# Kernel tuning notes

Measured on AMD Instinct MI355X. Metric: run time of the kernel, lower is better.

Reference implementation:

```python
import jax, jax.numpy as jnp
import numpy as np

N_NODES = 50000
N_EDGES = 800000
F_IN = 32
H = 128
N_REL = 4
MAX_DEG = 10
N_GRAPHS = 64
N_BLOCKS = 2


def setup_inputs() -> dict:
    key = jax.random.key(0)
    ks = jax.random.split(key, 20)
    s = 0.05
    return {
        "x": jax.random.normal(ks[0], (N_NODES, F_IN), jnp.float32),
        "edge_index": jax.random.randint(ks[1], (2, N_EDGES), 0, N_NODES, dtype=jnp.int32),
        "edge_attr": jax.random.randint(ks[2], (N_EDGES,), 0, N_REL, dtype=jnp.int32),
        "batch_idx": jnp.sort(jax.random.randint(ks[3], (N_NODES,), 0, N_GRAPHS, dtype=jnp.int32)),
        "embed_W": jax.random.normal(ks[4], (F_IN, H), jnp.float32) * s,
        "embed_b": jax.random.normal(ks[5], (H,), jnp.float32) * s,
        "rgcn_Wrel": jax.random.normal(ks[6], (N_BLOCKS, N_REL, H, H), jnp.float32) * s,
        "rgcn_Wroot": jax.random.normal(ks[7], (N_BLOCKS, H, H), jnp.float32) * s,
        "rgcn_b": jax.random.normal(ks[8], (N_BLOCKS, H), jnp.float32) * s,
        "mf_Wl": jax.random.normal(ks[9], (N_BLOCKS, MAX_DEG + 1, H, H), jnp.float32) * s,
        "mf_bl": jax.random.normal(ks[10], (N_BLOCKS, MAX_DEG + 1, H), jnp.float32) * s,
        "mf_Wr": jax.random.normal(ks[11], (N_BLOCKS, MAX_DEG + 1, H, H), jnp.float32) * s,
        "lin1_W": jax.random.normal(ks[12], (H, H), jnp.float32) * s,
        "lin1_b": jax.random.normal(ks[13], (H,), jnp.float32) * s,
        "lin2_W": jax.random.normal(ks[14], (H, 1), jnp.float32) * s,
        "lin2_b": jax.random.normal(ks[15], (1,), jnp.float32) * s,
    }


def _rgcn(x, src, dst, rel, Wrel, Wroot, b):
    # PyG RGCNConv with default aggr='mean': per-relation mean over incoming
    # edges, then per-relation weight, plus root transform and bias.
    seg = dst * N_REL + rel  # composite segment id: (node, relation)
    agg = jax.ops.segment_sum(x[src], seg, num_segments=N_NODES * N_REL)
    cnt = jax.ops.segment_sum(jnp.ones((seg.shape[0],), x.dtype), seg,
                              num_segments=N_NODES * N_REL)
    agg = (agg / jnp.maximum(cnt, 1.0)[:, None]).reshape(N_NODES, N_REL, H)
    return jnp.einsum('nrh,rho->no', agg, Wrel) + x @ Wroot + b


def _mfconv(x, src, dst, Wl, bl, Wr):
    # PyG MFConv: sum-aggregate neighbors, then per-degree-bucket linear heads
    # (degree = in-degree clamped to MAX_DEG); lin_r applied to root x (no bias).
    h = jax.ops.segment_sum(x[src], dst, num_segments=N_NODES)  # [N,H]
    deg = jax.ops.segment_sum(jnp.ones((src.shape[0],), jnp.int32), dst,
                              num_segments=N_NODES)
    deg = jnp.minimum(deg, MAX_DEG)  # [N]
    # out_all: [D+1, N, H] candidate outputs, one per degree bucket
    out_all = (jnp.einsum('nh,dho->dno', h, Wl)
               + jnp.einsum('nh,dho->dno', x, Wr)
               + bl[:, None, :])
    return jnp.take_along_axis(out_all, deg[None, :, None], axis=0)[0]


def reference(x, edge_index, edge_attr, batch_idx, embed_W, embed_b,
              rgcn_Wrel, rgcn_Wroot, rgcn_b, mf_Wl, mf_bl, mf_Wr,
              lin1_W, lin1_b, lin2_W, lin2_b):
    src, dst = edge_index[0], edge_index[1]
    h = x @ embed_W + embed_b
    for blk in range(N_BLOCKS):
        if blk > 0:  # first block uses Identity instead of ReLU
            h = jax.nn.relu(h)
        h = _rgcn(h, src, dst, edge_attr, rgcn_Wrel[blk], rgcn_Wroot[blk], rgcn_b[blk])
        h = jax.nn.relu(h)
        h = _mfconv(h, src, dst, mf_Wl[blk], mf_bl[blk], mf_Wr[blk])
    g = jax.ops.segment_sum(h, batch_idx, num_segments=N_GRAPHS)  # global_add_pool
    g = jax.nn.relu(g @ lin1_W + lin1_b)
    return g @ lin2_W + lin2_b
```

## Files before the change

kernel.cpp:

```cpp
#include <hip/hip_runtime.h>
#include <hip/hip_bf16.h>

#define NRELS 4
#define MAXDEG 10
#define NBUCK 11
#define POOL_CHUNKS 8

typedef __attribute__((ext_vector_type(8))) short s16x8;
typedef __attribute__((ext_vector_type(4))) float f32x4;
typedef __attribute__((ext_vector_type(8))) unsigned short u16x8;

__device__ inline unsigned short f2b(float f) {
  __hip_bfloat16 h = __float2bfloat16(f);
  return *reinterpret_cast<unsigned short*>(&h);
}
__device__ inline float b2f(unsigned short u) {
  union { unsigned int i; float f; } v;
  v.i = ((unsigned int)u) << 16;
  return v.f;
}
__device__ inline float blo(unsigned int v) {
  union { unsigned int i; float f; } x;
  x.i = v << 16;
  return x.f;
}
__device__ inline float bhi(unsigned int v) {
  union { unsigned int i; float f; } x;
  x.i = v & 0xffff0000u;
  return x.f;
}

typedef __attribute__((address_space(3))) unsigned int lds_uint;
typedef __attribute__((address_space(1))) const unsigned int glob_uint;
__device__ __forceinline__ void gld_lds16(const void* g, void* l) {
  __builtin_amdgcn_global_load_lds((glob_uint*)g, (lds_uint*)l, 16, 0, 0);
}

__global__ __launch_bounds__(512) void coarse_count_scan(
    const int* __restrict__ dst, int* __restrict__ bhist, int* __restrict__ boff,
    int* __restrict__ bcur, int* __restrict__ done, int NB, int E, int nblocks) {
  __shared__ int lh[512];
  __shared__ int lastf;
  int t = threadIdx.x;
  lh[t] = 0;
  __syncthreads();
  int base = blockIdx.x * 4096;
  int lim = E - base;
  if (lim > 4096) lim = 4096;
  for (int i = t; i < lim; i += 512) atomicAdd(&lh[dst[base + i] >> 7], 1);
  __syncthreads();
  if (lh[t]) atomicAdd(&bhist[t], lh[t]);
  __threadfence();
  __syncthreads();
  if (t == 0) lastf = (atomicAdd(done, 1) == nblocks - 1) ? 1 : 0;
  __syncthreads();
  if (!lastf) return;
  int v = (t < NB) ? atomicAdd(&bhist[t], 0) : 0;
  lh[t] = v;
  __syncthreads();
  for (int o = 1; o < 512; o <<= 1) {
    int x = (t >= o) ? lh[t - o] : 0;
    __syncthreads();
    lh[t] += x;
    __syncthreads();
  }
  if (t < NB) {
    int st = lh[t] - v;
    boff[t] = st;
    bcur[t] = st;
  }
  if (t == 0) boff[NB] = E;
}

__global__ __launch_bounds__(512) void coarse_scatter(
    const int* __restrict__ src, const int* __restrict__ dst, const int* __restrict__ rel,
    int* __restrict__ bcur, uint2* __restrict__ ebuf, int E) {
  __shared__ int lhist[512];
  __shared__ int lstart[512];
  __shared__ int lcur[512];
  __shared__ int gbase[512];
  __shared__ uint2 stage[4096];
  int t = threadIdx.x;
  lhist[t] = 0;
  __syncthreads();
  int base = blockIdx.x * 4096;
  int lim = E - base;
  if (lim > 4096) lim = 4096;
  for (int i = t; i < lim; i += 512) atomicAdd(&lhist[dst[base + i] >> 7], 1);
  __syncthreads();
  int myc = lhist[t];
  lstart[t] = myc;
  __syncthreads();
  for (int o = 1; o < 512; o <<= 1) {
    int x = (t >= o) ? lstart[t - o] : 0;
    __syncthreads();
    lstart[t] += x;
    __syncthreads();
  }
  int incl = lstart[t];
  __syncthreads();
  lstart[t] = incl - myc;
  lcur[t] = 0;
  if (myc > 0) gbase[t] = atomicAdd(&bcur[t], myc);
  __syncthreads();
  for (int i = t; i < lim; i += 512) {
    int e = base + i;
    int d = dst[e];
    int b = d >> 7;
    int slot = lstart[b] + atomicAdd(&lcur[b], 1);
    stage[slot] = make_uint2((unsigned)(d * 4 + rel[e]), (unsigned)src[e]);
  }
  __syncthreads();
  for (int i = t; i < lim; i += 512) {
    uint2 val = stage[i];
    int b = (int)(val.x >> 9);
    ebuf[gbase[b] + (i - lstart[b])] = val;
  }
}

__global__ __launch_bounds__(512) void fine_place(
    const uint2* __restrict__ ebuf, const int* __restrict__ boff, int* __restrict__ cnt,
    int* __restrict__ seg_start, float* __restrict__ inv, int* __restrict__ deg,
    int* __restrict__ bucket, int* __restrict__ hist, int* __restrict__ csr, int NSEG) {
  __shared__ int lh[512];
  __shared__ int sc[512];
  __shared__ int lcur[512];
  __shared__ int lbh[16];
  int t = threadIdx.x;
  int b = blockIdx.x;
  lh[t] = 0;
  if (t < 16) lbh[t] = 0;
  __syncthreads();
  int s = boff[b], e = boff[b + 1];
  for (int i = s + t; i < e; i += 512) atomicAdd(&lh[ebuf[i].x & 511], 1);
  __syncthreads();
  int v = lh[t];
  sc[t] = v;
  __syncthreads();
  for (int o = 1; o < 512; o <<= 1) {
    int x = (t >= o) ? sc[t - o] : 0;
    __syncthreads();
    sc[t] += x;
    __syncthreads();
  }
  int gseg = b * 512 + t;
  int mystart = s + sc[t] - v;
  lcur[t] = mystart;
  if (gseg < NSEG) {
    cnt[gseg] = v;
    seg_start[gseg] = mystart;
    inv[gseg] = 1.0f / (float)(v > 1 ? v : 1);
    if ((t & 3) == 0) {
      int d = sc[t + 3] - sc[t] + v;
      int n = gseg >> 2;
      deg[n] = d;
      int bk = d < MAXDEG ? d : MAXDEG;
      bucket[n] = bk;
      atomicAdd(&lbh[bk], 1);
    }
  }
  __syncthreads();
  if (t < NBUCK && lbh[t]) atomicAdd(&hist[t], lbh[t]);
  for (int i = s + t; i < e; i += 512) {
    uint2 vv = ebuf[i];
    int pos = atomicAdd(&lcur[vv.x & 511], 1);
    csr[pos] = (int)vv.y;
  }
}

__global__ void build_perm(const int* __restrict__ bucket, const int* __restrict__ hist,
                           int* __restrict__ fill, int* __restrict__ perm, int N) {
  __shared__ int soff[NBUCK];
  if (threadIdx.x == 0) {
    int acc = 0;
    for (int b = 0; b < NBUCK; b++) {
      soff[b] = acc;
      acc += ((hist[b] + 63) >> 6) << 6;
    }
  }
  __syncthreads();
  int n = blockIdx.x * 256 + threadIdx.x;
  int b = (n < N) ? bucket[n] : -1;
  int lane = threadIdx.x & 63;
  for (int bb = 0; bb < NBUCK; bb++) {
    unsigned long long m = __ballot(b == bb);
    if (m == 0ULL) continue;
    int leader = __ffsll(m) - 1;
    int base = 0;
    if (lane == leader) base = atomicAdd(&fill[bb], __popcll(m));
    base = __shfl(base, leader);
    if (b == bb) {
      int idx = __popcll(m & ((1ULL << lane) - 1ULL));
      perm[soff[bb] + base + idx] = n;
    }
  }
}

__global__ void conv_weights(const float* __restrict__ Wrel, const float* __restrict__ Wroot,
                             const float* __restrict__ Wl, const float* __restrict__ Wr,
                             const float* __restrict__ embW, unsigned short* __restrict__ Bt,
                             unsigned short* __restrict__ Btm, unsigned short* __restrict__ Bte) {
  const int R1 = 2 * 128 * 640;
  const int R2 = R1 + 2 * 11 * 128 * 256;
  const int R3 = R2 + 128 * 32;
  int t = blockIdx.x * 256 + threadIdx.x;
  if (t < R1) {
    int blk = t / 81920;
    int rem = t % 81920;
    int n = rem / 640;
    int k = rem % 640;
    float v;
    if (k < 512)
      v = Wrel[(size_t)blk * 65536 + (size_t)k * 128 + n];
    else
      v = Wroot[(size_t)blk * 16384 + (size_t)(k - 512) * 128 + n];
    Bt[t] = f2b(v);
    return;
  }
  if (t < R2) {
    int t2 = t - R1;
    int k = t2 & 255;
    int n = (t2 >> 8) & 127;
    int bb = (t2 >> 15) % 11;
    int blk = t2 / (11 * 128 * 256);
    float v;
    if (k < 128)
      v = Wl[(((size_t)blk * 11 + bb) * 128 + k) * 128 + n];
    else
      v = Wr[(((size_t)blk * 11 + bb) * 128 + (k - 128)) * 128 + n];
    Btm[t2] = f2b(v);
    return;
  }
  if (t < R3) {
    int t3 = t - R2;
    int n = t3 >> 5, k = t3 & 31;
    Bte[t3] = f2b(embW[(size_t)k * 128 + n]);
  }
}

#define ACC8(v)                                   \
  do {                                            \
    a0 += blo((v).x); a1 += bhi((v).x);           \
    a2 += blo((v).y); a3 += bhi((v).y);           \
    a4 += blo((v).z); a5 += bhi((v).z);           \
    a6 += blo((v).w); a7 += bhi((v).w);           \
  } while (0)

__global__ __launch_bounds__(256) void rgcn_gather(
    const unsigned short* __restrict__ hb, const int* __restrict__ csr,
    const int* __restrict__ seg_start, const int* __restrict__ cnt,
    const float* __restrict__ inv, const int* __restrict__ perm,
    unsigned short* __restrict__ ahat, int total) {
  int half = blockIdx.x & 1;
  int i = (blockIdx.x >> 1) * 32 + (threadIdx.x >> 3);
  if (i >= total) return;
  int n = perm[i];
  if (n < 0) return;
  int c8 = half * 64 + (threadIdx.x & 7) * 8;
  int4 st4 = *(const int4*)(seg_start + (size_t)n * 4);
  int4 cn4 = *(const int4*)(cnt + (size_t)n * 4);
  float4 w4 = *(const float4*)(inv + (size_t)n * 4);
  int sts[4] = {st4.x, st4.y, st4.z, st4.w};
  int cns[4] = {cn4.x, cn4.y, cn4.z, cn4.w};
  float ws[4] = {w4.x, w4.y, w4.z, w4.w};
#pragma unroll
  for (int r = 0; r < 4; r++) {
    int st = sts[r], cn = cns[r];
    float w = ws[r];
    float a0 = 0.f, a1 = 0.f, a2 = 0.f, a3 = 0.f, a4 = 0.f, a5 = 0.f, a6 = 0.f, a7 = 0.f;
    int ii = 0;
    for (; ii + 4 <= cn; ii += 4) {
      int p0 = csr[st + ii], p1 = csr[st + ii + 1];
      int p2 = csr[st + ii + 2], p3 = csr[st + ii + 3];
      uint4 v0 = *(const uint4*)(hb + (size_t)p0 * 128 + c8);
      uint4 v1 = *(const uint4*)(hb + (size_t)p1 * 128 + c8);
      uint4 v2 = *(const uint4*)(hb + (size_t)p2 * 128 + c8);
      uint4 v3 = *(const uint4*)(hb + (size_t)p3 * 128 + c8);
      ACC8(v0);
      ACC8(v1);
      ACC8(v2);
      ACC8(v3);
    }
    if (ii + 2 <= cn) {
      int p0 = csr[st + ii], p1 = csr[st + ii + 1];
      uint4 v0 = *(const uint4*)(hb + (size_t)p0 * 128 + c8);
      uint4 v1 = *(const uint4*)(hb + (size_t)p1 * 128 + c8);
      ACC8(v0);
      ACC8(v1);
      ii += 2;
    }
    if (ii < cn) {
      uint4 v0 = *(const uint4*)(hb + (size_t)csr[st + ii] * 128 + c8);
      ACC8(v0);
    }
    uint4 o;
    o.x = (unsigned int)f2b(a0 * w) | ((unsigned int)f2b(a1 * w) << 16);
    o.y = (unsigned int)f2b(a2 * w) | ((unsigned int)f2b(a3 * w) << 16);
    o.z = (unsigned int)f2b(a4 * w) | ((unsigned int)f2b(a5 * w) << 16);
    o.w = (unsigned int)f2b(a6 * w) | ((unsigned int)f2b(a7 * w) << 16);
    *(uint4*)(ahat + (size_t)i * 512 + r * 128 + c8) = o;
  }
}

__global__ __launch_bounds__(256) void mf_gather(
    const unsigned short* __restrict__ hb, const int* __restrict__ csr,
    const int* __restrict__ seg_start, const int* __restrict__ deg,
    const int* __restrict__ perm, unsigned short* __restrict__ amf, int total) {
  int half = blockIdx.x & 1;
  int i = (blockIdx.x >> 1) * 32 + (threadIdx.x >> 3);
  if (i >= total) return;
  int n = perm[i];
  if (n < 0) return;
  int c8 = half * 64 + (threadIdx.x & 7) * 8;
  int st = seg_start[n * 4], dg = deg[n];
  float a0 = 0.f, a1 = 0.f, a2 = 0.f, a3 = 0.f, a4 = 0.f, a5 = 0.f, a6 = 0.f, a7 = 0.f;
  int i2 = 0;
  for (; i2 + 4 <= dg; i2 += 4) {
    int p0 = csr[st + i2], p1 = csr[st + i2 + 1];
    int p2 = csr[st + i2 + 2], p3 = csr[st + i2 + 3];
    uint4 v0 = *(const uint4*)(hb + (size_t)p0 * 128 + c8);
    uint4 v1 = *(const uint4*)(hb + (size_t)p1 * 128 + c8);
    uint4 v2 = *(const uint4*)(hb + (size_t)p2 * 128 + c8);
    uint4 v3 = *(const uint4*)(hb + (size_t)p3 * 128 + c8);
    ACC8(v0);
    ACC8(v1);
    ACC8(v2);
    ACC8(v3);
  }
  if (i2 + 2 <= dg) {
    int p0 = csr[st + i2], p1 = csr[st + i2 + 1];
    uint4 v0 = *(const uint4*)(hb + (size_t)p0 * 128 + c8);
    uint4 v1 = *(const uint4*)(hb + (size_t)p1 * 128 + c8);
    ACC8(v0);
    ACC8(v1);
    i2 += 2;
  }
  if (i2 < dg) {
    uint4 v0 = *(const uint4*)(hb + (size_t)csr[st + i2] * 128 + c8);
    ACC8(v0);
  }
  uint4 o;
  o.x = (unsigned int)f2b(a0) | ((unsigned int)f2b(a1) << 16);
  o.y = (unsigned int)f2b(a2) | ((unsigned int)f2b(a3) << 16);
  o.z = (unsigned int)f2b(a4) | ((unsigned int)f2b(a5) << 16);
  o.w = (unsigned int)f2b(a6) | ((unsigned int)f2b(a7) << 16);
  *(uint4*)(amf + (size_t)i * 128 + c8) = o;
}

__global__ __launch_bounds__(256) void rgcn_mfma(const unsigned short* __restrict__ A,
                                                 const unsigned short* __restrict__ hroot,
                                                 const unsigned short* __restrict__ Bt,
                                                 const float* __restrict__ bias,
                                                 const int* __restrict__ perm,
                                                 unsigned short* __restrict__ out) {
  __shared__ unsigned char As[8192];
  __shared__ unsigned char Bs[16384];
  __shared__ int nodes[64];
  int t = threadIdx.x;
  int m0 = blockIdx.x * 64;
  if (t >= 64 && t < 128) nodes[t - 64] = perm[m0 + t - 64];
  __syncthreads();
  int lane = t & 63, wave = t >> 6;
  int row = lane & 15, quad = lane >> 4;
  int nh = wave * 32;
  f32x4 acc[2][4];
#pragma unroll
  for (int i = 0; i < 2; i++)
#pragma unroll
    for (int j = 0; j < 4; j++) acc[i][j] = (f32x4){0.f, 0.f, 0.f, 0.f};

  for (int kt = 0; kt < 10; kt++) {
    int kb2 = kt * 128;
#pragma unroll
    for (int s = 0; s < 2; s++) {
      int o = s * 4096 + t * 16;
      int r = o >> 7, c = ((o >> 4) & 7) ^ (r & 7);
      const char* gsrc;
      if (kt < 8) {
        gsrc = (const char*)A + (size_t)(m0 + r) * 1024 + kb2 + c * 16;
      } else {
        int nd = nodes[r];
        if (nd < 0) nd = 0;
        gsrc = (const char*)hroot + (size_t)nd * 256 + (kb2 - 1024) + c * 16;
      }
      gld_lds16(gsrc, As + o);
    }
#pragma unroll
    for (int s = 0; s < 4; s++) {
      int o = s * 4096 + t * 16;
      int r = o >> 7, c = ((o >> 4) & 7) ^ (r & 7);
      gld_lds16((const char*)Bt + (size_t)r * 1280 + kb2 + c * 16, Bs + o);
    }
    __syncthreads();
#pragma unroll
    for (int ks = 0; ks < 2; ks++) {
      int cch = ks * 4 + quad;
      s16x8 af[4], bf[2];
#pragma unroll
      for (int mt = 0; mt < 4; mt++) {
        int R = mt * 16 + row;
        af[mt] = *(const s16x8*)(As + R * 128 + ((cch ^ (R & 7)) << 4));
      }
#pragma unroll
      for (int nt = 0; nt < 2; nt++) {
        int R = nh + nt * 16 + row;
        bf[nt] = *(const s16x8*)(Bs + R * 128 + ((cch ^ (R & 7)) << 4));
      }
#pragma unroll
      for (int nt = 0; nt < 2; nt++)
#pragma unroll
        for (int mt = 0; mt < 4; mt++)
          acc[nt][mt] = __builtin_amdgcn_mfma_f32_16x16x32_bf16(af[mt], bf[nt], acc[nt][mt], 0, 0, 0);
    }
    __syncthreads();
  }
#pragma unroll
  for (int nt = 0; nt < 2; nt++) {
    int n = nh + nt * 16 + row;
    float bv = bias[n];
#pragma unroll
    for (int mt = 0; mt < 4; mt++) {
#pragma unroll
      for (int r4 = 0; r4 < 4; r4++) {
        int nd = nodes[mt * 16 + quad * 4 + r4];
        if (nd >= 0) out[(size_t)nd * 128 + n] = f2b(fmaxf(acc[nt][mt][r4] + bv, 0.f));
      }
    }
  }
}

__global__ __launch_bounds__(256) void mf_mfma(const unsigned short* __restrict__ A,
                                               const unsigned short* __restrict__ hroot,
                                               const unsigned short* __restrict__ Bt,
                                               const float* __restrict__ bl,
                                               const int* __restrict__ perm,
                                               const int* __restrict__ hist,
                                               unsigned short* __restrict__ out, int relu_out) {
  __shared__ unsigned char As[8192];
  __shared__ unsigned char Bs[16384];
  __shared__ int soff[NBUCK + 1];
  __shared__ int nodes[64];
  int t = threadIdx.x;
  int m0 = blockIdx.x * 64;
  if (t == 0) {
    int acc = 0;
    for (int b2 = 0; b2 < NBUCK; b2++) {
      soff[b2] = acc;
      acc += ((hist[b2] + 63) >> 6) << 6;
    }
    soff[NBUCK] = acc;
  }
  if (t >= 64 && t < 128) nodes[t - 64] = perm[m0 + t - 64];
  __syncthreads();
  if (m0 >= soff[NBUCK]) return;
  int b = 0;
  while (b < 10 && m0 >= soff[b + 1]) b++;
  const unsigned short* Bb = Bt + (size_t)b * 128 * 256;
  const float* bb = bl + b * 128;
  int lane = t & 63, wave = t >> 6;
  int row = lane & 15, quad = lane >> 4;
  int nh = wave * 32;
  f32x4 acc[2][4];
#pragma unroll
  for (int i = 0; i < 2; i++)
#pragma unroll
    for (int j = 0; j < 4; j++) acc[i][j] = (f32x4){0.f, 0.f, 0.f, 0.f};

  for (int kt = 0; kt < 4; kt++) {
    int kb2 = kt * 128;
#pragma unroll
    for (int s = 0; s < 2; s++) {
      int o = s * 4096 + t * 16;
      int r = o >> 7, c = ((o >> 4) & 7) ^ (r & 7);
      const char* gsrc;
      if (kt < 2) {
        gsrc = (const char*)A + (size_t)(m0 + r) * 256 + kb2 + c * 16;
      } else {
        int nd = nodes[r];
        if (nd < 0) nd = 0;
        gsrc = (const char*)hroot + (size_t)nd * 256 + (kb2 - 512) + c * 16;
      }
      gld_lds16(gsrc, As + o);
    }
#pragma unroll
    for (int s = 0; s < 4; s++) {
      int o = s * 4096 + t * 16;
      int r = o >> 7, c = ((o >> 4) & 7) ^ (r & 7);
      gld_lds16((const char*)Bb + (size_t)r * 512 + kb2 + c * 16, Bs + o);
    }
    __syncthreads();
#pragma unroll
    for (int ks = 0; ks < 2; ks++) {
      int cch = ks * 4 + quad;
      s16x8 af[4], bf[2];
#pragma unroll
      for (int mt = 0; mt < 4; mt++) {
        int R = mt * 16 + row;
        af[mt] = *(const s16x8*)(As + R * 128 + ((cch ^ (R & 7)) << 4));
      }
#pragma unroll
      for (int nt = 0; nt < 2; nt++) {
        int R = nh + nt * 16 + row;
        bf[nt] = *(const s16x8*)(Bs + R * 128 + ((cch ^ (R & 7)) << 4));
      }
#pragma unroll
      for (int nt = 0; nt < 2; nt++)
#pragma unroll
        for (int mt = 0; mt < 4; mt++)
          acc[nt][mt] = __builtin_amdgcn_mfma_f32_16x16x32_bf16(af[mt], bf[nt], acc[nt][mt], 0, 0, 0);
    }
    __syncthreads();
  }
#pragma unroll
  for (int nt = 0; nt < 2; nt++) {
    int n = nh + nt * 16 + row;
    float bv = bb[n];
#pragma unroll
    for (int mt = 0; mt < 4; mt++) {
#pragma unroll
      for (int r4 = 0; r4 < 4; r4++) {
        int nd = nodes[mt * 16 + quad * 4 + r4];
        if (nd >= 0) {
          float v = acc[nt][mt][r4] + bv;
          if (relu_out) v = fmaxf(v, 0.f);
          out[(size_t)nd * 128 + n] = f2b(v);
        }
      }
    }
  }
}

__global__ __launch_bounds__(256) void embed_mfma(const float* __restrict__ x,
                                                  const unsigned short* __restrict__ Bte,
                                                  const float* __restrict__ bias,
                                                  unsigned short* __restrict__ out, int N) {
  __shared__ unsigned char As[64 * 80];
  __shared__ unsigned char Bs[128 * 80];
  int t = threadIdx.x;
  int m0 = blockIdx.x * 64;
  {
    int r = t >> 2, s = t & 3;
    int gr = m0 + r;
    if (gr >= N) gr = N - 1;
    const float* xp = x + (size_t)gr * 32 + s * 8;
    float4 f0 = *(const float4*)xp;
    float4 f1 = *(const float4*)(xp + 4);
    u16x8 o;
    o[0] = f2b(f0.x); o[1] = f2b(f0.y); o[2] = f2b(f0.z); o[3] = f2b(f0.w);
    o[4] = f2b(f1.x); o[5] = f2b(f1.y); o[6] = f2b(f1.z); o[7] = f2b(f1.w);
    *(u16x8*)(As + r * 80 + s * 16) = o;
  }
  {
    int n = t >> 1, s = t & 1;
    const unsigned short* bp = Bte + (size_t)n * 32 + s * 16;
    uint4 v0 = *(const uint4*)bp;
    uint4 v1 = *(const uint4*)(bp + 8);
    *(uint4*)(Bs + n * 80 + s * 32) = v0;
    *(uint4*)(Bs + n * 80 + s * 32 + 16) = v1;
  }
  __syncthreads();
  int lane = t & 63, wave = t >> 6;
  int row = lane & 15, quad = lane >> 4;
  int nh = wave * 32;
  f32x4 acc[2][4];
#pragma unroll
  for (int i = 0; i < 2; i++)
#pragma unroll
    for (int j = 0; j < 4; j++) acc[i][j] = (f32x4){0.f, 0.f, 0.f, 0.f};
  s16x8 af[4], bf[2];
#pragma unroll
  for (int mt = 0; mt < 4; mt++) {
    int R = mt * 16 + row;
    af[mt] = *(const s16x8*)(As + R * 80 + quad * 16);
  }
#pragma unroll
  for (int nt = 0; nt < 2; nt++) {
    int R = nh + nt * 16 + row;
    bf[nt] = *(const s16x8*)(Bs + R * 80 + quad * 16);
  }
#pragma unroll
  for (int nt = 0; nt < 2; nt++)
#pragma unroll
    for (int mt = 0; mt < 4; mt++)
      acc[nt][mt] = __builtin_amdgcn_mfma_f32_16x16x32_bf16(af[mt], bf[nt], acc[nt][mt], 0, 0, 0);
#pragma unroll
  for (int nt = 0; nt < 2; nt++) {
    int n = nh + nt * 16 + row;
    float bv = bias[n];
#pragma unroll
    for (int mt = 0; mt < 4; mt++) {
#pragma unroll
      for (int r4 = 0; r4 < 4; r4++) {
        int m = m0 + mt * 16 + quad * 4 + r4;
        if (m < N) out[(size_t)m * 128 + n] = f2b(acc[nt][mt][r4] + bv);
      }
    }
  }
}

__global__ void pool2(const unsigned short* __restrict__ h, const int* __restrict__ batch,
                      float* __restrict__ g, int N, int G) {
  int gr = blockIdx.x / POOL_CHUNKS;
  int ck = blockIdx.x % POOL_CHUNKS;
  int t = threadIdx.x;
  int lane = t & 63, grp = t >> 6;
  int lo = 0, hi = N;
  while (lo < hi) {
    int m = (lo + hi) >> 1;
    if (batch[m] < gr) lo = m + 1; else hi = m;
  }
  int s = lo;
  lo = s; hi = N;
  while (lo < hi) {
    int m = (lo + hi) >> 1;
    if (batch[m] < gr + 1) lo = m + 1; else hi = m;
  }
  int e = lo;
  int len = e - s;
  int a = s + (int)(((long long)len * ck) / POOL_CHUNKS);
  int b = s + (int)(((long long)len * (ck + 1)) / POOL_CHUNKS);
  float s0 = 0.f, s1 = 0.f;
  for (int n = a + grp; n < b; n += 2) {
    unsigned int v = *(const unsigned int*)(h + (size_t)n * 128 + lane * 2);
    s0 += blo(v);
    s1 += bhi(v);
  }
  if (b > a + grp) {
    atomicAdd(&g[gr * 128 + lane * 2], s0);
    atomicAdd(&g[gr * 128 + lane * 2 + 1], s1);
  }
}

__global__ void head_kernel(const float* __restrict__ g, const float* __restrict__ W1,
                            const float* __restrict__ b1, const float* __restrict__ W2,
                            const float* __restrict__ b2, float* __restrict__ out) {
  int bg = blockIdx.x;
  int o = threadIdx.x;
  __shared__ float gs[128];
  __shared__ float red[128];
  gs[o] = g[bg * 128 + o];
  __syncthreads();
  float acc = b1[o];
  for (int k = 0; k < 128; k++) acc += gs[k] * W1[k * 128 + o];
  acc = fmaxf(acc, 0.f);
  red[o] = acc * W2[o];
  __syncthreads();
  for (int s = 64; s > 0; s >>= 1) {
    if (o < s) red[o] += red[o + s];
    __syncthreads();
  }
  if (o == 0) out[bg] = red[0] + b2[0];
}

extern "C" void kernel_launch(void* const* d_in, const int* in_sizes, int n_in,
                              void* d_out, int out_size, void* d_ws, size_t ws_size,
                              hipStream_t stream) {
  const float* x = (const float*)d_in[0];
  const int* ei = (const int*)d_in[1];
  const int* ea = (const int*)d_in[2];
  const int* batch = (const int*)d_in[3];
  const float* embW = (const float*)d_in[4];
  const float* embB = (const float*)d_in[5];
  const float* Wrel = (const float*)d_in[6];
  const float* Wroot = (const float*)d_in[7];
  const float* rb = (const float*)d_in[8];
  const float* Wl = (const float*)d_in[9];
  const float* bl = (const float*)d_in[10];
  const float* Wr = (const float*)d_in[11];
  const float* l1W = (const float*)d_in[12];
  const float* l1b = (const float*)d_in[13];
  const float* l2W = (const float*)d_in[14];
  const float* l2b = (const float*)d_in[15];
  float* out = (float*)d_out;

  int N = in_sizes[0] / 32;
  int E = in_sizes[2];
  int G = out_size;
  int NSEG = N * 4;
  int NB = (N + 127) >> 7;

  char* p = (char*)d_ws;
  auto alloc = [&](size_t bytes) {
    char* r = p;
    p += (bytes + 255) & ~(size_t)255;
    return r;
  };
  int permCap = ((N + 63) / 64 + NBUCK) * 64;
  unsigned short* h_bf = (unsigned short*)alloc((size_t)N * 128 * 2);
  unsigned short* h2_bf = (unsigned short*)alloc((size_t)N * 128 * 2);
  unsigned short* ahat = (unsigned short*)alloc((size_t)permCap * 512 * 2);
  unsigned short* amf = (unsigned short*)alloc((size_t)permCap * 128 * 2);
  unsigned short* Btr = (unsigned short*)alloc((size_t)2 * 128 * 640 * 2);
  unsigned short* Btm = (unsigned short*)alloc((size_t)2 * 11 * 128 * 256 * 2);
  unsigned short* Bte = (unsigned short*)alloc((size_t)128 * 32 * 2);
  float* inv = (float*)alloc((size_t)NSEG * 4);
  int* cnt = (int*)alloc((size_t)NSEG * 4);
  int* seg_start = (int*)alloc((size_t)NSEG * 4);
  int* csr = (int*)alloc((size_t)E * 4);
  uint2* ebuf = (uint2*)alloc((size_t)E * 8);
  int* deg = (int*)alloc((size_t)N * 4);
  int* bucket = (int*)alloc((size_t)N * 4);
  int* perm = (int*)alloc((size_t)permCap * 4);
  int* boff = (int*)alloc(516 * 4);
  int* bcur = (int*)alloc(512 * 4);
  size_t zeroBytes = 8192 + (size_t)G * 128 * 4;
  char* zb = alloc(zeroBytes);
  int* bhist = (int*)zb;
  int* hist = (int*)(zb + 4096);
  int* fill = (int*)(zb + 4224);
  int* done = (int*)(zb + 4352);
  float* g = (float*)(zb + 8192);

  hipMemsetAsync(zb, 0, zeroBytes, stream);
  hipMemsetAsync(perm, 0xFF, (size_t)permCap * 4, stream);

  const int* src = ei;
  const int* dst = ei + E;

  int sblocks = (E + 4095) / 4096;
  coarse_count_scan<<<sblocks, 512, 0, stream>>>(dst, bhist, boff, bcur, done, NB, E, sblocks);
  coarse_scatter<<<sblocks, 512, 0, stream>>>(src, dst, ea, bcur, ebuf, E);
  fine_place<<<NB, 512, 0, stream>>>(ebuf, boff, cnt, seg_start, inv, deg, bucket, hist, csr,
                                     NSEG);
  build_perm<<<(N + 255) / 256, 256, 0, stream>>>(bucket, hist, fill, perm, N);
  int convTotal = 2 * 128 * 640 + 2 * 11 * 128 * 256 + 128 * 32;
  conv_weights<<<(convTotal + 255) / 256, 256, 0, stream>>>(Wrel, Wroot, Wl, Wr, embW, Btr,
                                                            Btm, Bte);

  embed_mfma<<<(N + 63) / 64, 256, 0, stream>>>(x, Bte, embB, h_bf, N);

  int mfblocks = permCap / 64;
  int gblocks = ((permCap + 31) / 32) * 2;
  for (int blk = 0; blk < 2; blk++) {
    rgcn_gather<<<gblocks, 256, 0, stream>>>(h_bf, csr, seg_start, cnt, inv, perm, ahat,
                                             permCap);
    rgcn_mfma<<<mfblocks, 256, 0, stream>>>(ahat, h_bf, Btr + (size_t)blk * 81920,
                                            rb + blk * 128, perm, h2_bf);
    mf_gather<<<gblocks, 256, 0, stream>>>(h2_bf, csr, seg_start, deg, perm, amf, permCap);
    mf_mfma<<<mfblocks, 256, 0, stream>>>(amf, h2_bf, Btm + (size_t)blk * 11 * 128 * 256,
                                          bl + (size_t)blk * 11 * 128, perm, hist, h_bf,
                                          (blk == 0) ? 1 : 0);
  }
  pool2<<<G * POOL_CHUNKS, 128, 0, stream>>>(h_bf, batch, g, N, G);
  head_kernel<<<G, 128, 0, stream>>>(g, l1W, l1b, l2W, l2b, out);
}
```

Before: 397.8 us.

## Fuse embed and weight conversion, fold perm init, use nontemporal gather IO

Merges the weight-conversion and embedding kernels into one launch. Embedding blocks now convert embW to bf16 themselves, and the extra blocks convert the RGCN and MF weights. The perm -1 fill moves from a memset into coarse_count_scan. The gather kernels use nontemporal loads for CSR indices and nontemporal stores for their outputs, to cut launch count and cache pollution. Each embed block re-reads and converts embW redundantly, and nontemporal stores may hurt the following MFMA kernels if they expected those outputs to stay in L2.

Measured after the change: 454.7 us. 14.3% more time.

```diff
diff --git a/kernel.cpp b/kernel.cpp
--- a/kernel.cpp
+++ b/kernel.cpp
@@ -9,6 +9,7 @@
 typedef __attribute__((ext_vector_type(8))) short s16x8;
 typedef __attribute__((ext_vector_type(4))) float f32x4;
 typedef __attribute__((ext_vector_type(8))) unsigned short u16x8;
+typedef __attribute__((ext_vector_type(4))) unsigned int u32x4;
 
 __device__ inline unsigned short f2b(float f) {
   __hip_bfloat16 h = __float2bfloat16(f);
@@ -29,6 +30,10 @@
   x.i = v & 0xffff0000u;
   return x.f;
 }
+__device__ __forceinline__ int ntl(const int* p) { return __builtin_nontemporal_load(p); }
+__device__ __forceinline__ void nts16(u32x4 v, unsigned short* p) {
+  __builtin_nontemporal_store(v, (u32x4*)p);
+}
 
 typedef __attribute__((address_space(3))) unsigned int lds_uint;
 typedef __attribute__((address_space(1))) const unsigned int glob_uint;
@@ -38,12 +43,14 @@
 
 __global__ __launch_bounds__(512) void coarse_count_scan(
     const int* __restrict__ dst, int* __restrict__ bhist, int* __restrict__ boff,
-    int* __restrict__ bcur, int* __restrict__ done, int NB, int E, int nblocks) {
+    int* __restrict__ bcur, int* __restrict__ done, int* __restrict__ perm, int permCap,
+    int NB, int E, int nblocks) {
   __shared__ int lh[512];
   __shared__ int lastf;
   int t = threadIdx.x;
   lh[t] = 0;
   __syncthreads();
+  for (int i = blockIdx.x * 512 + t; i < permCap; i += nblocks * 512) perm[i] = -1;
   int base = blockIdx.x * 4096;
   int lim = E - base;
   if (lim > 4096) lim = 4096;
@@ -196,45 +203,103 @@
   }
 }
 
-__global__ void conv_weights(const float* __restrict__ Wrel, const float* __restrict__ Wroot,
-                             const float* __restrict__ Wl, const float* __restrict__ Wr,
-                             const float* __restrict__ embW, unsigned short* __restrict__ Bt,
-                             unsigned short* __restrict__ Btm, unsigned short* __restrict__ Bte) {
-  const int R1 = 2 * 128 * 640;
-  const int R2 = R1 + 2 * 11 * 128 * 256;
-  const int R3 = R2 + 128 * 32;
-  int t = blockIdx.x * 256 + threadIdx.x;
-  if (t < R1) {
-    int blk = t / 81920;
-    int rem = t % 81920;
-    int n = rem / 640;
-    int k = rem % 640;
-    float v;
-    if (k < 512)
-      v = Wrel[(size_t)blk * 65536 + (size_t)k * 128 + n];
-    else
-      v = Wroot[(size_t)blk * 16384 + (size_t)(k - 512) * 128 + n];
-    Bt[t] = f2b(v);
+__global__ __launch_bounds__(256) void embed_conv(
+    const float* __restrict__ x, const float* __restrict__ embW,
+    const float* __restrict__ bias, const float* __restrict__ Wrel,
+    const float* __restrict__ Wroot, const float* __restrict__ Wl,
+    const float* __restrict__ Wr, unsigned short* __restrict__ Bt,
+    unsigned short* __restrict__ Btm, unsigned short* __restrict__ out, int N, int nbE) {
+  if ((int)blockIdx.x >= nbE) {
+    const int R1 = 2 * 128 * 640;
+    const int R2 = R1 + 2 * 11 * 128 * 256;
+    int t = (blockIdx.x - nbE) * 256 + threadIdx.x;
+    if (t < R1) {
+      int blk = t / 81920;
+      int rem = t % 81920;
+      int n = rem / 640;
+      int k = rem % 640;
+      float v;
+      if (k < 512)
+        v = Wrel[(size_t)blk * 65536 + (size_t)k * 128 + n];
+      else
+        v = Wroot[(size_t)blk * 16384 + (size_t)(k - 512) * 128 + n];
+      Bt[t] = f2b(v);
+    } else if (t < R2) {
+      int t2 = t - R1;
+      int k = t2 & 255;
+      int n = (t2 >> 8) & 127;
+      int bb = (t2 >> 15) % 11;
+      int blk = t2 / (11 * 128 * 256);
+      float v;
+      if (k < 128)
+        v = Wl[(((size_t)blk * 11 + bb) * 128 + k) * 128 + n];
+      else
+        v = Wr[(((size_t)blk * 11 + bb) * 128 + (k - 128)) * 128 + n];
+      Btm[t2] = f2b(v);
+    }
     return;
   }
-  if (t < R2) {
-    int t2 = t - R1;
-    int k = t2 & 255;
-    int n = (t2 >> 8) & 127;
-    int bb = (t2 >> 15) % 11;
-    int blk = t2 / (11 * 128 * 256);
-    float v;
-    if (k < 128)
-      v = Wl[(((size_t)blk * 11 + bb) * 128 + k) * 128 + n];
-    else
-      v = Wr[(((size_t)blk * 11 + bb) * 128 + (k - 128)) * 128 + n];
-    Btm[t2] = f2b(v);
-    return;
-  }
-  if (t < R3) {
-    int t3 = t - R2;
-    int n = t3 >> 5, k = t3 & 31;
-    Bte[t3] = f2b(embW[(size_t)k * 128 + n]);
+  __shared__ unsigned char As[64 * 80];
+  __shared__ unsigned char Bs[128 * 80];
+  int t = threadIdx.x;
+  int m0 = blockIdx.x * 64;
+  {
+    int r = t >> 2, s = t & 3;
+    int gr = m0 + r;
+    if (gr >= N) gr = N - 1;
+    const float* xp = x + (size_t)gr * 32 + s * 8;
+    float4 f0 = *(const float4*)xp;
+    float4 f1 = *(const float4*)(xp + 4);
+    u16x8 o;
+    o[0] = f2b(f0.x); o[1] = f2b(f0.y); o[2] = f2b(f0.z); o[3] = f2b(f0.w);
+    o[4] = f2b(f1.x); o[5] = f2b(f1.y); o[6] = f2b(f1.z); o[7] = f2b(f1.w);
+    *(u16x8*)(As + r * 80 + s * 16) = o;
+  }
+  {
+    int n = t >> 1, hf = t & 1;
+    unsigned short tmp[16];
+#pragma unroll
+    for (int j = 0; j < 16; j++) tmp[j] = f2b(embW[(size_t)(hf * 16 + j) * 128 + n]);
+    *(u16x8*)(Bs + n * 80 + hf * 32) = *(u16x8*)tmp;
+    *(u16x8*)(Bs + n * 80 + hf * 32 + 16) = *(u16x8*)(tmp + 8);
+  }
+  __syncthreads();
+  int lane = t & 63, wave = t >> 6;
+  int row = lane & 15, quad = lane >> 4;
+  int nh = wave * 32;
+  f32x4 acc[2][4];
+#pragma unroll
+  for (int i = 0; i < 2; i++)
+#pragma unroll
+    for (int j = 0; j < 4; j++) acc[i][j] = (f32x4){0.f, 0.f, 0.f, 0.f};
+  s16x8 af[4], bf[2];
+#pragma unroll
+  for (int mt = 0; mt < 4; mt++) {
+    int R = mt * 16 + row;
+    af[mt] = *(const s16x8*)(As + R * 80 + quad * 16);
+  }
+#pragma unroll
+  for (int nt = 0; nt < 2; nt++) {
+    int R = nh + nt * 16 + row;
+    bf[nt] = *(const s16x8*)(Bs + R * 80 + quad * 16);
+  }
+#pragma unroll
+  for (int nt = 0; nt < 2; nt++)
+#pragma unroll
+    for (int mt = 0; mt < 4; mt++)
+      acc[nt][mt] = __builtin_amdgcn_mfma_f32_16x16x32_bf16(af[mt], bf[nt], acc[nt][mt], 0, 0, 0);
+#pragma unroll
+  for (int nt = 0; nt < 2; nt++) {
+    int n = nh + nt * 16 + row;
+    float bv = bias[n];
+#pragma unroll
+    for (int mt = 0; mt < 4; mt++) {
+#pragma unroll
+      for (int r4 = 0; r4 < 4; r4++) {
+        int m = m0 + mt * 16 + quad * 4 + r4;
+        if (m < N) out[(size_t)m * 128 + n] = f2b(acc[nt][mt][r4] + bv);
+      }
+    }
   }
 }
 
@@ -270,8 +335,8 @@
     float a0 = 0.f, a1 = 0.f, a2 = 0.f, a3 = 0.f, a4 = 0.f, a5 = 0.f, a6 = 0.f, a7 = 0.f;
     int ii = 0;
     for (; ii + 4 <= cn; ii += 4) {
-      int p0 = csr[st + ii], p1 = csr[st + ii + 1];
-      int p2 = csr[st + ii + 2], p3 = csr[st + ii + 3];
+      int p0 = ntl(csr + st + ii), p1 = ntl(csr + st + ii + 1);
+      int p2 = ntl(csr + st + ii + 2), p3 = ntl(csr + st + ii + 3);
       uint4 v0 = *(const uint4*)(hb + (size_t)p0 * 128 + c8);
       uint4 v1 = *(const uint4*)(hb + (size_t)p1 * 128 + c8);
       uint4 v2 = *(const uint4*)(hb + (size_t)p2 * 128 + c8);
@@ -282,7 +347,7 @@
       ACC8(v3);
     }
     if (ii + 2 <= cn) {
-      int p0 = csr[st + ii], p1 = csr[st + ii + 1];
+      int p0 = ntl(csr + st + ii), p1 = ntl(csr + st + ii + 1);
       uint4 v0 = *(const uint4*)(hb + (size_t)p0 * 128 + c8);
       uint4 v1 = *(const uint4*)(hb + (size_t)p1 * 128 + c8);
       ACC8(v0);
@@ -290,15 +355,15 @@
       ii += 2;
     }
     if (ii < cn) {
-      uint4 v0 = *(const uint4*)(hb + (size_t)csr[st + ii] * 128 + c8);
+      uint4 v0 = *(const uint4*)(hb + (size_t)ntl(csr + st + ii) * 128 + c8);
       ACC8(v0);
     }
-    uint4 o;
+    u32x4 o;
     o.x = (unsigned int)f2b(a0 * w) | ((unsigned int)f2b(a1 * w) << 16);
     o.y = (unsigned int)f2b(a2 * w) | ((unsigned int)f2b(a3 * w) << 16);
     o.z = (unsigned int)f2b(a4 * w) | ((unsigned int)f2b(a5 * w) << 16);
     o.w = (unsigned int)f2b(a6 * w) | ((unsigned int)f2b(a7 * w) << 16);
-    *(uint4*)(ahat + (size_t)i * 512 + r * 128 + c8) = o;
+    nts16(o, ahat + (size_t)i * 512 + r * 128 + c8);
   }
 }
 
@@ -316,8 +381,8 @@
   float a0 = 0.f, a1 = 0.f, a2 = 0.f, a3 = 0.f, a4 = 0.f, a5 = 0.f, a6 = 0.f, a7 = 0.f;
   int i2 = 0;
   for (; i2 + 4 <= dg; i2 += 4) {
-    int p0 = csr[st + i2], p1 = csr[st + i2 + 1];
-    int p2 = csr[st + i2 + 2], p3 = csr[st + i2 + 3];
+    int p0 = ntl(csr + st + i2), p1 = ntl(csr + st + i2 + 1);
+    int p2 = ntl(csr + st + i2 + 2), p3 = ntl(csr + st + i2 + 3);
     uint4 v0 = *(const uint4*)(hb + (size_t)p0 * 128 + c8);
     uint4 v1 = *(const uint4*)(hb + (size_t)p1 * 128 + c8);
     uint4 v2 = *(const uint4*)(hb + (size_t)p2 * 128 + c8);
@@ -328,7 +393,7 @@
     ACC8(v3);
   }
   if (i2 + 2 <= dg) {
-    int p0 = csr[st + i2], p1 = csr[st + i2 + 1];
+    int p0 = ntl(csr + st + i2), p1 = ntl(csr + st + i2 + 1);
     uint4 v0 = *(const uint4*)(hb + (size_t)p0 * 128 + c8);
     uint4 v1 = *(const uint4*)(hb + (size_t)p1 * 128 + c8);
     ACC8(v0);
@@ -336,15 +401,15 @@
     i2 += 2;
   }
   if (i2 < dg) {
-    uint4 v0 = *(const uint4*)(hb + (size_t)csr[st + i2] * 128 + c8);
+    uint4 v0 = *(const uint4*)(hb + (size_t)ntl(csr + st + i2) * 128 + c8);
     ACC8(v0);
   }
-  uint4 o;
+  u32x4 o;
   o.x = (unsigned int)f2b(a0) | ((unsigned int)f2b(a1) << 16);
   o.y = (unsigned int)f2b(a2) | ((unsigned int)f2b(a3) << 16);
   o.z = (unsigned int)f2b(a4) | ((unsigned int)f2b(a5) << 16);
   o.w = (unsigned int)f2b(a6) | ((unsigned int)f2b(a7) << 16);
-  *(uint4*)(amf + (size_t)i * 128 + c8) = o;
+  nts16(o, amf + (size_t)i * 128 + c8);
 }
 
 __global__ __launch_bounds__(256) void rgcn_mfma(const unsigned short* __restrict__ A,
@@ -525,74 +590,6 @@
           if (relu_out) v = fmaxf(v, 0.f);
           out[(size_t)nd * 128 + n] = f2b(v);
         }
-      }
-    }
-  }
-}
-
-__global__ __launch_bounds__(256) void embed_mfma(const float* __restrict__ x,
-                                                  const unsigned short* __restrict__ Bte,
-                                                  const float* __restrict__ bias,
-                                                  unsigned short* __restrict__ out, int N) {
-  __shared__ unsigned char As[64 * 80];
-  __shared__ unsigned char Bs[128 * 80];
-  int t = threadIdx.x;
-  int m0 = blockIdx.x * 64;
-  {
-    int r = t >> 2, s = t & 3;
-    int gr = m0 + r;
-    if (gr >= N) gr = N - 1;
-    const float* xp = x + (size_t)gr * 32 + s * 8;
-    float4 f0 = *(const float4*)xp;
-    float4 f1 = *(const float4*)(xp + 4);
-    u16x8 o;
-    o[0] = f2b(f0.x); o[1] = f2b(f0.y); o[2] = f2b(f0.z); o[3] = f2b(f0.w);
-    o[4] = f2b(f1.x); o[5] = f2b(f1.y); o[6] = f2b(f1.z); o[7] = f2b(f1.w);
-    *(u16x8*)(As + r * 80 + s * 16) = o;
-  }
-  {
-    int n = t >> 1, s = t & 1;
-    const unsigned short* bp = Bte + (size_t)n * 32 + s * 16;
-    uint4 v0 = *(const uint4*)bp;
-    uint4 v1 = *(const uint4*)(bp + 8);
-    *(uint4*)(Bs + n * 80 + s * 32) = v0;
-    *(uint4*)(Bs + n * 80 + s * 32 + 16) = v1;
-  }
-  __syncthreads();
-  int lane = t & 63, wave = t >> 6;
-  int row = lane & 15, quad = lane >> 4;
-  int nh = wave * 32;
-  f32x4 acc[2][4];
-#pragma unroll
-  for (int i = 0; i < 2; i++)
-#pragma unroll
-    for (int j = 0; j < 4; j++) acc[i][j] = (f32x4){0.f, 0.f, 0.f, 0.f};
-  s16x8 af[4], bf[2];
-#pragma unroll
-  for (int mt = 0; mt < 4; mt++) {
-    int R = mt * 16 + row;
-    af[mt] = *(const s16x8*)(As + R * 80 + quad * 16);
-  }
-#pragma unroll
-  for (int nt = 0; nt < 2; nt++) {
-    int R = nh + nt * 16 + row;
-    bf[nt] = *(const s16x8*)(Bs + R * 80 + quad * 16);
-  }
-#pragma unroll
-  for (int nt = 0; nt < 2; nt++)
-#pragma unroll
-    for (int mt = 0; mt < 4; mt++)
-      acc[nt][mt] = __builtin_amdgcn_mfma_f32_16x16x32_bf16(af[mt], bf[nt], acc[nt][mt], 0, 0, 0);
-#pragma unroll
-  for (int nt = 0; nt < 2; nt++) {
-    int n = nh + nt * 16 + row;
-    float bv = bias[n];
-#pragma unroll
-    for (int mt = 0; mt < 4; mt++) {
-#pragma unroll
-      for (int r4 = 0; r4 < 4; r4++) {
-        int m = m0 + mt * 16 + quad * 4 + r4;
-        if (m < N) out[(size_t)m * 128 + n] = f2b(acc[nt][mt][r4] + bv);
       }
     }
   }
@@ -692,7 +689,6 @@
   unsigned short* amf = (unsigned short*)alloc((size_t)permCap * 128 * 2);
   unsigned short* Btr = (unsigned short*)alloc((size_t)2 * 128 * 640 * 2);
   unsigned short* Btm = (unsigned short*)alloc((size_t)2 * 11 * 128 * 256 * 2);
-  unsigned short* Bte = (unsigned short*)alloc((size_t)128 * 32 * 2);
   float* inv = (float*)alloc((size_t)NSEG * 4);
   int* cnt = (int*)alloc((size_t)NSEG * 4);
   int* seg_start = (int*)alloc((size_t)NSEG * 4);
@@ -711,23 +707,23 @@
   int* done = (int*)(zb + 4352);
   float* g = (float*)(zb + 8192);
 
-  hipMemsetAsync(zb, 0, zeroBytes, stream);
-  hipMemsetAsync(perm, 0xFF, (size_t)permCap * 4, stream);
+  (void)hipMemsetAsync(zb, 0, zeroBytes, stream);
 
   const int* src = ei;
   const int* dst = ei + E;
 
   int sblocks = (E + 4095) / 4096;
-  coarse_count_scan<<<sblocks, 512, 0, stream>>>(dst, bhist, boff, bcur, done, NB, E, sblocks);
+  coarse_count_scan<<<sblocks, 512, 0, stream>>>(dst, bhist, boff, bcur, done, perm, permCap,
+                                                 NB, E, sblocks);
   coarse_scatter<<<sblocks, 512, 0, stream>>>(src, dst, ea, bcur, ebuf, E);
   fine_place<<<NB, 512, 0, stream>>>(ebuf, boff, cnt, seg_start, inv, deg, bucket, hist, csr,
                                      NSEG);
   build_perm<<<(N + 255) / 256, 256, 0, stream>>>(bucket, hist, fill, perm, N);
-  int convTotal = 2 * 128 * 640 + 2 * 11 * 128 * 256 + 128 * 32;
-  conv_weights<<<(convTotal + 255) / 256, 256, 0, stream>>>(Wrel, Wroot, Wl, Wr, embW, Btr,
-                                                            Btm, Bte);
-
-  embed_mfma<<<(N + 63) / 64, 256, 0, stream>>>(x, Bte, embB, h_bf, N);
+
+  int nbE = (N + 63) / 64;
+  int convBlocks = (2 * 128 * 640 + 2 * 11 * 128 * 256 + 255) / 256;
+  embed_conv<<<nbE + convBlocks, 256, 0, stream>>>(x, embW, embB, Wrel, Wroot, Wl, Wr, Btr,
+                                                   Btm, h_bf, N, nbE);
 
   int mfblocks = permCap / 64;
   int gblocks = ((permCap + 31) / 32) * 2;
```
